# Optimization experiments

Measured on AMD Instinct MI355X. Metric: run time of the kernel, lower is better.

Reference implementation:

```python
import jax, jax.numpy as jnp
import numpy as np

B, H, W, C, NUM_HEADS = 32, 8, 128, 512, 8
HK, WK = 7, 11  # local_k
N = H * W
HEAD_DIM = C // NUM_HEADS
SCALE = HEAD_DIM ** (-0.5)


def make_local_mask():
    # key (i,j) is visible to query (h,w) iff i+HK//2 in [h, h+HK) and j+WK//2 in [w, w+WK)
    dh = jnp.arange(H)[None, :] - jnp.arange(H)[:, None] + HK // 2  # [H(query), H(key)]
    dw = jnp.arange(W)[None, :] - jnp.arange(W)[:, None] + WK // 2  # [W(query), W(key)]
    ok_h = (dh >= 0) & (dh < HK)
    ok_w = (dw >= 0) & (dw < WK)
    ok = ok_h[:, None, :, None] & ok_w[None, :, None, :]  # [H,W,H,W]
    return jnp.where(ok.reshape(N, N), 0.0, -jnp.inf).astype(jnp.float32)


def setup_inputs() -> dict:
    key = jax.random.key(0)
    k1, k2, k3 = jax.random.split(key, 3)
    s = C ** (-0.5)
    return {
        "x": jax.random.normal(k1, (B, N, C), dtype=jnp.float32),
        "w_qkv": jax.random.normal(k2, (C, 3 * C), dtype=jnp.float32) * s,
        "w_proj": jax.random.normal(k3, (C, C), dtype=jnp.float32) * s,
        "b_proj": jnp.zeros((C,), dtype=jnp.float32),
    }


def reference(x, w_qkv, w_proj, b_proj):
    mask = make_local_mask()  # [N, N], 0 in window, -inf outside
    b, n, c = x.shape
    qkv = (x @ w_qkv).reshape(b, n, 3, NUM_HEADS, HEAD_DIM)
    qkv = jnp.transpose(qkv, (2, 0, 3, 1, 4))  # [3, B, heads, N, head_dim]
    q, k, v = qkv[0], qkv[1], qkv[2]
    attn = jnp.einsum('bhqd,bhkd->bhqk', q, k) * SCALE + mask
    attn = jax.nn.softmax(attn, axis=-1)
    out = jnp.einsum('bhqk,bhkd->bhqd', attn, v)
    out = jnp.transpose(out, (0, 2, 1, 3)).reshape(b, n, c)
    return out @ w_proj + b_proj
```

## Files before the change

kernel.cpp:

```cpp
#include <hip/hip_runtime.h>

#define Bsz   32
#define Hh    8
#define Ww    128
#define Cc    512
#define NHEAD 8
#define HD    64
#define NN    1024
#define SCALE 0.125f
#define ROWS  1536
#define ROWSP 1568

typedef _Float16 f16x8 __attribute__((ext_vector_type(8)));
typedef float    f32x4 __attribute__((ext_vector_type(4)));

__device__ __forceinline__ void gload16(const _Float16* g, _Float16* l) {
#if __has_builtin(__builtin_amdgcn_global_load_lds)
  __builtin_amdgcn_global_load_lds(
      (const __attribute__((address_space(1))) unsigned int*)g,
      (__attribute__((address_space(3))) unsigned int*)l, 16, 0, 0);
#else
  *(uint4*)l = *(const uint4*)g;
#endif
}

__global__ __launch_bounds__(256) void cvt_f32_f16(
    const float* __restrict__ in, _Float16* __restrict__ out, int n8) {
  const int i = blockIdx.x * 256 + threadIdx.x;
  if (i < n8) {
    const float4 f0 = ((const float4*)in)[(size_t)i * 2];
    const float4 f1 = ((const float4*)in)[(size_t)i * 2 + 1];
    union { _Float16 h[8]; uint4 u; } pk;
    pk.h[0] = (_Float16)f0.x; pk.h[1] = (_Float16)f0.y;
    pk.h[2] = (_Float16)f0.z; pk.h[3] = (_Float16)f0.w;
    pk.h[4] = (_Float16)f1.x; pk.h[5] = (_Float16)f1.y;
    pk.h[6] = (_Float16)f1.z; pk.h[7] = (_Float16)f1.w;
    ((uint4*)out)[i] = pk.u;
  }
}

__global__ __launch_bounds__(256) void tcvt(
    const float* __restrict__ in, _Float16* __restrict__ out, int Nn, int K) {
  const int id = blockIdx.x * 256 + threadIdx.x;
  if (id < Nn * K) {
    const int n = id / K, k = id - n * K;
    out[id] = (_Float16)in[(size_t)k * Nn + n];
  }
}

template<bool OUT_F16, bool HAS_BIAS>
__global__ __launch_bounds__(512, 4) void gemm_mfma(
    const _Float16* __restrict__ A,
    const _Float16* __restrict__ BT,
    const float* __restrict__ bias,
    void* __restrict__ Cout,
    int nbx, int Nn, int K, int ldc)
{
  __shared__ _Float16 As[2][128 * 32];
  __shared__ _Float16 Bs[2][256 * 32];

  const int wg    = blockIdx.x;
  const int chunk = gridDim.x >> 3;
  const int nid   = (wg & 7) * chunk + (wg >> 3);
  const int bn    = (nid % nbx) * 256;
  const int bm    = (nid / nbx) * 128;

  const int t  = threadIdx.x;
  const int l  = t & 63, wv = t >> 6;
  const int wr = wv >> 2, wc = wv & 3;

  f32x4 acc[4][4] = {};

  const int arow = t >> 2;
  const int ac   = (t & 3) * 8;

  auto stage = [&](int k0, int pb) {
    gload16(A  + (size_t)(bm + arow)       * K + k0 + ac, &As[pb][arow * 32 + ac]);
    gload16(BT + (size_t)(bn + arow)       * K + k0 + ac, &Bs[pb][arow * 32 + ac]);
    gload16(BT + (size_t)(bn + 128 + arow) * K + k0 + ac, &Bs[pb][(128 + arow) * 32 + ac]);
  };

  const int nt = K / 32;

  stage(0, 0);
  __syncthreads();

  int buf = 0;
  for (int tt = 0; tt < nt; ++tt) {
    if (tt + 1 < nt) stage((tt + 1) * 32, buf ^ 1);

    const int rA = l & 15, ks = (l >> 4) * 8;
    f16x8 aF[4], bF[4];
#pragma unroll
    for (int i = 0; i < 4; ++i)
      aF[i] = *(const f16x8*)&As[buf][(wr * 64 + i * 16 + rA) * 32 + ks];
#pragma unroll
    for (int j = 0; j < 4; ++j)
      bF[j] = *(const f16x8*)&Bs[buf][(wc * 64 + j * 16 + rA) * 32 + ks];
#pragma unroll
    for (int i = 0; i < 4; ++i)
#pragma unroll
      for (int j = 0; j < 4; ++j)
        acc[i][j] = __builtin_amdgcn_mfma_f32_16x16x32_f16(aF[i], bF[j], acc[i][j], 0, 0, 0);

    __syncthreads();
    buf ^= 1;
  }

  const int lc = l & 15, lr4 = (l >> 4) * 4;
#pragma unroll
  for (int i = 0; i < 4; ++i) {
    const size_t row0 = (size_t)(bm + wr * 64 + i * 16 + lr4);
#pragma unroll
    for (int j = 0; j < 4; ++j) {
      const int col = bn + wc * 64 + j * 16 + lc;
      const float bv = HAS_BIAS ? bias[col] : 0.f;
#pragma unroll
      for (int r = 0; r < 4; ++r) {
        const float v = acc[i][j][r] + bv;
        if (OUT_F16)
          ((_Float16*)Cout)[(row0 + r) * ldc + col] = (_Float16)v;
        else
          ((float*)Cout)[(row0 + r) * ldc + col] = v;
      }
    }
  }
}

__global__ __launch_bounds__(512, 4) void local_attn_mfma(
    const _Float16* __restrict__ qkv, _Float16* __restrict__ outh)
{
  const int wg  = blockIdx.x;
  const int nid = ((wg & 7) << 7) + (wg >> 3);
  const int hp = nid & 3, head = (nid >> 2) & 7, b = nid >> 5;
  const int h0 = hp * 2;

  const int t = threadIdx.x;
  const int wv = t >> 6, l = t & 63;
  const int g = l >> 4, c = l & 15;
  const int w0 = wv * 16;
  const int kb = min(max(w0 - 8, 0), 96);

  __shared__ _Float16 Ksh[8192];
  __shared__ _Float16 Vsh[64 * 132];
  __shared__ _Float16 Pbuf[8][576];

  const _Float16* qb = qkv + (size_t)b * NN * ROWSP;

  f16x8 qF[2][2];
#pragma unroll
  for (int hi = 0; hi < 2; ++hi) {
    const _Float16* Qg = qb + (size_t)((h0 + hi) * Ww + w0 + c) * ROWSP + head * HD;
    qF[hi][0] = *(const f16x8*)&Qg[g * 8];
    qF[hi][1] = *(const f16x8*)&Qg[32 + g * 8];
  }

  float mbias[2][4];
#pragma unroll
  for (int tt = 0; tt < 2; ++tt)
#pragma unroll
    for (int r = 0; r < 4; ++r) {
      const int kcol = kb + 16 * tt + 4 * g + r;
      const int qq   = w0 + c;
      mbias[tt][r] = (kcol >= qq - 5 && kcol <= qq + 5) ? 0.f : -1e30f;
    }

  const int r0 = max(0, h0 - 3), r1 = min(Hh - 1, h0 + 4);
  float s_part[2] = {0.f, 0.f};
  f32x4 accO[2][4] = {};

  const int dd = t & 7, cg = (t & 255) >> 3;

  for (int kr = r0; kr <= r1; ++kr) {
    __syncthreads();
    if (t < 256) {
      const _Float16* Kg = qb + (size_t)(kr * Ww) * ROWSP + Cc + head * HD;
#pragma unroll
      for (int i = 0; i < 4; ++i) {
        const int o   = (i * 4 + wv) * 64 + l;
        const int col = o >> 3, dc = o & 7;
        gload16(Kg + (size_t)col * ROWSP + ((dc ^ (col & 7)) << 3), &Ksh[o * 8]);
      }
    } else {
      f16x8 vr[4];
      const _Float16* Vg = qb + (size_t)(kr * Ww + cg * 4) * ROWSP + 2 * Cc + head * HD + dd * 8;
#pragma unroll
      for (int i = 0; i < 4; ++i)
        vr[i] = *(const f16x8*)&Vg[(size_t)i * ROWSP];
#pragma unroll
      for (int e = 0; e < 8; ++e) {
        union { _Float16 hh[4]; uint2 u; } pk;
        pk.hh[0] = vr[0][e]; pk.hh[1] = vr[1][e];
        pk.hh[2] = vr[2][e]; pk.hh[3] = vr[3][e];
        *(uint2*)&Vsh[(dd * 8 + e) * 132 + cg * 4] = pk.u;
      }
    }
    __syncthreads();

#pragma unroll
    for (int hi = 0; hi < 2; ++hi) {
      const int hq = h0 + hi;
      if (kr < hq - 3 || kr > hq + 3) continue;

      f32x4 accS[2] = {};
      __builtin_amdgcn_s_setprio(1);
#pragma unroll
      for (int tt = 0; tt < 2; ++tt) {
        const int col = kb + 16 * tt + c;
#pragma unroll
        for (int s = 0; s < 2; ++s) {
          const f16x8 kF = *(const f16x8*)&Ksh[col * 64 + (((s * 4 + g) ^ (c & 7)) << 3)];
          accS[tt] = __builtin_amdgcn_mfma_f32_16x16x32_f16(kF, qF[hi][s], accS[tt], 0, 0, 0);
        }
      }
      __builtin_amdgcn_s_setprio(0);

#pragma unroll
      for (int tt = 0; tt < 2; ++tt) {
        float p0 = __expf(fminf(__builtin_fmaf(accS[tt][0], SCALE, mbias[tt][0]), 11.f));
        float p1 = __expf(fminf(__builtin_fmaf(accS[tt][1], SCALE, mbias[tt][1]), 11.f));
        float p2 = __expf(fminf(__builtin_fmaf(accS[tt][2], SCALE, mbias[tt][2]), 11.f));
        float p3 = __expf(fminf(__builtin_fmaf(accS[tt][3], SCALE, mbias[tt][3]), 11.f));
        s_part[hi] += (p0 + p1) + (p2 + p3);
        union { _Float16 hh[4]; uint2 u; } pk;
        pk.hh[0] = (_Float16)p0; pk.hh[1] = (_Float16)p1;
        pk.hh[2] = (_Float16)p2; pk.hh[3] = (_Float16)p3;
        *(uint2*)&Pbuf[wv][c * 36 + 16 * tt + 4 * g] = pk.u;
      }

      union { f16x8 v; uint2 u2[2]; } pF;
      {
        const _Float16* pp = &Pbuf[wv][c * 36 + g * 8];
        pF.u2[0] = *(const uint2*)pp;
        pF.u2[1] = *(const uint2*)(pp + 4);
      }
      __builtin_amdgcn_s_setprio(1);
#pragma unroll
      for (int jj = 0; jj < 4; ++jj) {
        union { f16x8 v; uint2 u2[2]; } vF;
        const _Float16* vp = &Vsh[(16 * jj + c) * 132 + kb + g * 8];
        vF.u2[0] = *(const uint2*)vp;
        vF.u2[1] = *(const uint2*)(vp + 4);
        accO[hi][jj] = __builtin_amdgcn_mfma_f32_16x16x32_f16(pF.v, vF.v, accO[hi][jj], 0, 0, 0);
      }
      __builtin_amdgcn_s_setprio(0);
    }
  }

#pragma unroll
  for (int hi = 0; hi < 2; ++hi) {
    float s_run = s_part[hi];
    s_run += __shfl_xor(s_run, 16);
    s_run += __shfl_xor(s_run, 32);
    _Float16* ob = outh + ((size_t)b * NN + (h0 + hi) * Ww + w0) * Cc + head * HD;
#pragma unroll
    for (int r = 0; r < 4; ++r) {
      const float sr  = __shfl(s_run, 4 * g + r, 16);
      const float inv = 1.f / sr;
      const int q = 4 * g + r;
#pragma unroll
      for (int jj = 0; jj < 4; ++jj)
        ob[(size_t)q * Cc + 16 * jj + c] = (_Float16)(accO[hi][jj][r] * inv);
    }
  }
}

extern "C" void kernel_launch(void* const* d_in, const int* in_sizes, int n_in,
                              void* d_out, int out_size, void* d_ws, size_t ws_size,
                              hipStream_t stream)
{
  const float* x      = (const float*)d_in[0];
  const float* w_qkv  = (const float*)d_in[1];
  const float* w_proj = (const float*)d_in[2];
  const float* b_proj = (const float*)d_in[3];
  float* out = (float*)d_out;

  const int M = Bsz * NN;
  char* ws = (char*)d_ws;
  _Float16* xh    = (_Float16*)ws;
  _Float16* qkvh  = (_Float16*)(ws + 33554432);
  _Float16* attnh = (_Float16*)(ws + 136314880);
  _Float16* wqT   = (_Float16*)(ws + 169869312);
  _Float16* wpT   = (_Float16*)(ws + 171442176);

  cvt_f32_f16<<<(M * Cc / 8 + 255) / 256, 256, 0, stream>>>(x, xh, M * Cc / 8);
  tcvt<<<(ROWS * Cc + 255) / 256, 256, 0, stream>>>(w_qkv, wqT, ROWS, Cc);
  tcvt<<<(Cc * Cc + 255) / 256, 256, 0, stream>>>(w_proj, wpT, Cc, Cc);

  gemm_mfma<true, false><<<(ROWS / 256) * (M / 128), 512, 0, stream>>>(
      xh, wqT, nullptr, qkvh, ROWS / 256, ROWS, Cc, ROWSP);

  local_attn_mfma<<<(Hh / 2) * NHEAD * Bsz, 512, 0, stream>>>(qkvh, attnh);

  gemm_mfma<false, true><<<(Cc / 256) * (M / 128), 512, 0, stream>>>(
      attnh, wpT, b_proj, out, Cc / 256, Cc, Cc, Cc);
}
```

Baseline: 167.8 us.

## Enlarge GEMM tile to 256x256 and swizzle LDS layout to avoid bank conflicts

The MFMA GEMM block tile grows from 128x256 to 256x256, so each wave now computes 128x64 with 8x4 accumulators, and the launch grids are halved to match. LDS staging now XOR-swizzles the k-chunk index by row, and fragment reads apply the same swizzle, to cut LDS bank conflicts. The aim is more reuse of each staged tile and cheaper LDS reads, at the cost of doubled accumulator registers, more LDS per block, lower occupancy (launch bound 2) and fewer blocks in the grid.

```diff
diff --git a/kernel.cpp b/kernel.cpp
--- a/kernel.cpp
+++ b/kernel.cpp
@@ -49,59 +49,62 @@
 }
 
 template<bool OUT_F16, bool HAS_BIAS>
-__global__ __launch_bounds__(512, 4) void gemm_mfma(
+__global__ __launch_bounds__(512, 2) void gemm_mfma(
     const _Float16* __restrict__ A,
     const _Float16* __restrict__ BT,
     const float* __restrict__ bias,
     void* __restrict__ Cout,
     int nbx, int Nn, int K, int ldc)
 {
-  __shared__ _Float16 As[2][128 * 32];
+  __shared__ _Float16 As[2][256 * 32];
   __shared__ _Float16 Bs[2][256 * 32];
 
   const int wg    = blockIdx.x;
   const int chunk = gridDim.x >> 3;
   const int nid   = (wg & 7) * chunk + (wg >> 3);
   const int bn    = (nid % nbx) * 256;
-  const int bm    = (nid / nbx) * 128;
+  const int bm    = (nid / nbx) * 256;
 
   const int t  = threadIdx.x;
   const int l  = t & 63, wv = t >> 6;
   const int wr = wv >> 2, wc = wv & 3;
 
-  f32x4 acc[4][4] = {};
-
-  const int arow = t >> 2;
-  const int ac   = (t & 3) * 8;
+  f32x4 acc[8][4] = {};
 
   auto stage = [&](int k0, int pb) {
-    gload16(A  + (size_t)(bm + arow)       * K + k0 + ac, &As[pb][arow * 32 + ac]);
-    gload16(BT + (size_t)(bn + arow)       * K + k0 + ac, &Bs[pb][arow * 32 + ac]);
-    gload16(BT + (size_t)(bn + 128 + arow) * K + k0 + ac, &Bs[pb][(128 + arow) * 32 + ac]);
+#pragma unroll
+    for (int q = 0; q < 2; ++q) {
+      const int c   = t + q * 512;
+      const int row = c >> 2, k4 = c & 3;
+      const int ks  = (k4 ^ ((row >> 1) & 3)) << 3;
+      gload16(A  + (size_t)(bm + row) * K + k0 + ks, &As[pb][c * 8]);
+      gload16(BT + (size_t)(bn + row) * K + k0 + ks, &Bs[pb][c * 8]);
+    }
   };
 
   const int nt = K / 32;
 
   stage(0, 0);
   __syncthreads();
+
+  const int rA   = l & 15;
+  const int kofs = ((l >> 4) * 8) ^ (((rA >> 1) & 3) << 3);
 
   int buf = 0;
   for (int tt = 0; tt < nt; ++tt) {
     if (tt + 1 < nt) stage((tt + 1) * 32, buf ^ 1);
 
-    const int rA = l & 15, ks = (l >> 4) * 8;
-    f16x8 aF[4], bF[4];
-#pragma unroll
-    for (int i = 0; i < 4; ++i)
-      aF[i] = *(const f16x8*)&As[buf][(wr * 64 + i * 16 + rA) * 32 + ks];
-#pragma unroll
-    for (int j = 0; j < 4; ++j)
-      bF[j] = *(const f16x8*)&Bs[buf][(wc * 64 + j * 16 + rA) * 32 + ks];
-#pragma unroll
-    for (int i = 0; i < 4; ++i)
-#pragma unroll
-      for (int j = 0; j < 4; ++j)
-        acc[i][j] = __builtin_amdgcn_mfma_f32_16x16x32_f16(aF[i], bF[j], acc[i][j], 0, 0, 0);
+    f16x8 bF[4];
+#pragma unroll
+    for (int jj = 0; jj < 4; ++jj)
+      bF[jj] = *(const f16x8*)&Bs[buf][(wc * 64 + jj * 16 + rA) * 32 + kofs];
+#pragma unroll
+    for (int i = 0; i < 8; ++i) {
+      const f16x8 aF = *(const f16x8*)&As[buf][(wr * 128 + i * 16 + rA) * 32 + kofs];
+#pragma unroll
+      for (int jj = 0; jj < 4; ++jj)
+        acc[i][jj] = __builtin_amdgcn_mfma_f32_16x16x32_f16(aF, bF[jj], acc[i][jj], 0, 0, 0);
+    }
 
     __syncthreads();
     buf ^= 1;
@@ -109,15 +112,15 @@
 
   const int lc = l & 15, lr4 = (l >> 4) * 4;
 #pragma unroll
-  for (int i = 0; i < 4; ++i) {
-    const size_t row0 = (size_t)(bm + wr * 64 + i * 16 + lr4);
-#pragma unroll
-    for (int j = 0; j < 4; ++j) {
-      const int col = bn + wc * 64 + j * 16 + lc;
+  for (int i = 0; i < 8; ++i) {
+    const size_t row0 = (size_t)(bm + wr * 128 + i * 16 + lr4);
+#pragma unroll
+    for (int jj = 0; jj < 4; ++jj) {
+      const int col = bn + wc * 64 + jj * 16 + lc;
       const float bv = HAS_BIAS ? bias[col] : 0.f;
 #pragma unroll
       for (int r = 0; r < 4; ++r) {
-        const float v = acc[i][j][r] + bv;
+        const float v = acc[i][jj][r] + bv;
         if (OUT_F16)
           ((_Float16*)Cout)[(row0 + r) * ldc + col] = (_Float16)v;
         else
@@ -287,11 +290,11 @@
   tcvt<<<(ROWS * Cc + 255) / 256, 256, 0, stream>>>(w_qkv, wqT, ROWS, Cc);
   tcvt<<<(Cc * Cc + 255) / 256, 256, 0, stream>>>(w_proj, wpT, Cc, Cc);
 
-  gemm_mfma<true, false><<<(ROWS / 256) * (M / 128), 512, 0, stream>>>(
+  gemm_mfma<true, false><<<(ROWS / 256) * (M / 256), 512, 0, stream>>>(
       xh, wqT, nullptr, qkvh, ROWS / 256, ROWS, Cc, ROWSP);
 
   local_attn_mfma<<<(Hh / 2) * NHEAD * Bsz, 512, 0, stream>>>(qkvh, attnh);
 
-  gemm_mfma<false, true><<<(Cc / 256) * (M / 128), 512, 0, stream>>>(
+  gemm_mfma<false, true><<<(Cc / 256) * (M / 256), 512, 0, stream>>>(
       attnh, wpT, b_proj, out, Cc / 256, Cc, Cc, Cc);
 }
```

New measurement: 183.5 us. +9.4%, slower.
